# Optimization experiments

Measured on AMD Instinct MI355X. Metric: run time of the kernel, lower is better.

The kernel has to match this reference:

```python
import jax, jax.numpy as jnp
import numpy as np

CROP_H, CROP_W = 14, 14
EXTRAP = 0.0


def setup_inputs() -> dict:
    key = jax.random.key(0)
    k1, k2, k3 = jax.random.split(key, 3)
    image = jax.random.normal(k1, (8, 256, 200, 200), dtype=jnp.float32)
    boxes = jax.random.uniform(k2, (512, 4), dtype=jnp.float32)  # normalized [y1,x1,y2,x2]
    box_indices = jax.random.randint(k3, (512,), 0, 8).astype(jnp.int32)
    return {"image": image, "boxes": boxes, "box_indices": box_indices}


def _crop_and_resize(image, boxes, box_indices, crop_h, crop_w, extrap):
    # TF-style crop_and_resize with bilinear sampling (matches crop_and_resize_cpu).
    B, C, H, W = image.shape
    N = boxes.shape[0]
    y1, x1, y2, x2 = boxes[:, 0], boxes[:, 1], boxes[:, 2], boxes[:, 3]
    h_scale = (y2 - y1) * (H - 1) / (crop_h - 1)
    w_scale = (x2 - x1) * (W - 1) / (crop_w - 1)
    in_y = y1[:, None] * (H - 1) + jnp.arange(crop_h, dtype=jnp.float32)[None, :] * h_scale[:, None]  # [N,ch]
    in_x = x1[:, None] * (W - 1) + jnp.arange(crop_w, dtype=jnp.float32)[None, :] * w_scale[:, None]  # [N,cw]
    valid_y = (in_y >= 0) & (in_y <= H - 1)  # [N,ch]
    valid_x = (in_x >= 0) & (in_x <= W - 1)  # [N,cw]

    y_floor = jnp.floor(in_y)
    x_floor = jnp.floor(in_x)
    ly = (in_y - y_floor)[:, :, None, None]  # [N,ch,1,1]
    lx = (in_x - x_floor)[:, None, :, None]  # [N,1,cw,1]
    y0 = jnp.clip(y_floor, 0, H - 1).astype(jnp.int32)
    y1i = jnp.clip(jnp.ceil(in_y), 0, H - 1).astype(jnp.int32)
    x0 = jnp.clip(x_floor, 0, W - 1).astype(jnp.int32)
    x1i = jnp.clip(jnp.ceil(in_x), 0, W - 1).astype(jnp.int32)

    b = box_indices.astype(jnp.int32)[:, None, None]  # [N,1,1]

    def gather(yi, xi):
        # advanced indices [N,ch,cw] separated by ':' slice -> result [N,ch,cw,C]
        return image[b, :, yi[:, :, None], xi[:, None, :]]

    tl = gather(y0, x0)
    tr = gather(y0, x1i)
    bl = gather(y1i, x0)
    br = gather(y1i, x1i)

    top = tl + (tr - tl) * lx
    bot = bl + (br - bl) * lx
    val = top + (bot - top) * ly  # [N,ch,cw,C]

    mask = (valid_y[:, :, None] & valid_x[:, None, :])[:, :, :, None]
    val = jnp.where(mask, val, jnp.float32(extrap))
    return jnp.transpose(val, (0, 3, 1, 2))  # [N,C,ch,cw]


def reference(image, boxes, box_indices):
    return _crop_and_resize(image, boxes, box_indices, CROP_H, CROP_W, EXTRAP)
```

## Files before the change

### kernel.cpp

```cpp
#include <hip/hip_runtime.h>

#define CROP_H 14
#define CROP_W 14
#define NBOX   512
#define CH     256
#define IMH    200
#define IMW    200
#define PER_BOX (CH * CROP_H * CROP_W)
#define BLOCKS_PER_BOX (PER_BOX / 256)

__global__ __launch_bounds__(256) void CropAndResize_60146722013533_kernel(
    const float* __restrict__ image,
    const float* __restrict__ boxes,
    const int*   __restrict__ box_idx,
    float*       __restrict__ out)
{
    const int n = blockIdx.x;
    const int t = threadIdx.x;

    __shared__ int   sy0[CROP_H], sy1[CROP_H], sx0[CROP_W], sx1[CROP_W];
    __shared__ float sly[CROP_H], slx[CROP_W];
    __shared__ int   svy[CROP_H], svx[CROP_W];
    __shared__ int   sb;

    if (t < CROP_H + CROP_W) {
        const float by1 = boxes[n * 4 + 0];
        const float bx1 = boxes[n * 4 + 1];
        const float by2 = boxes[n * 4 + 2];
        const float bx2 = boxes[n * 4 + 3];
        if (t < CROP_H) {
            const int gy = t;
            float h_scale = (by2 - by1) * (float)(IMH - 1) / (float)(CROP_H - 1);
            float in_y = by1 * (float)(IMH - 1) + (float)gy * h_scale;
            svy[gy] = (in_y >= 0.0f && in_y <= (float)(IMH - 1)) ? 1 : 0;
            float yf = floorf(in_y);
            sly[gy] = in_y - yf;
            sy0[gy] = (int)fminf(fmaxf(yf, 0.0f), (float)(IMH - 1));
            sy1[gy] = (int)fminf(fmaxf(ceilf(in_y), 0.0f), (float)(IMH - 1));
        } else {
            const int gx = t - CROP_H;
            float w_scale = (bx2 - bx1) * (float)(IMW - 1) / (float)(CROP_W - 1);
            float in_x = bx1 * (float)(IMW - 1) + (float)gx * w_scale;
            svx[gx] = (in_x >= 0.0f && in_x <= (float)(IMW - 1)) ? 1 : 0;
            float xf = floorf(in_x);
            slx[gx] = in_x - xf;
            sx0[gx] = (int)fminf(fmaxf(xf, 0.0f), (float)(IMW - 1));
            sx1[gx] = (int)fminf(fmaxf(ceilf(in_x), 0.0f), (float)(IMW - 1));
        }
    }
    if (t == 0) sb = box_idx[n];
    __syncthreads();

    const int elem = blockIdx.y * 256 + t;
    const int c  = elem / (CROP_H * CROP_W);
    const int r  = elem - c * (CROP_H * CROP_W);
    const int gy = r / CROP_W;
    const int gx = r - gy * CROP_W;

    const float* base = image + ((size_t)(sb * CH + c)) * (size_t)(IMH * IMW);
    const int y0  = sy0[gy];
    const int y1i = sy1[gy];
    const int x0  = sx0[gx];
    const int x1i = sx1[gx];
    const float ly = sly[gy];
    const float lx = slx[gx];

    const int xb = (x0 < IMW - 2) ? x0 : (IMW - 2);
    const float* rowt = base + y0  * IMW + xb;
    const float* rowb = base + y1i * IMW + xb;
    float2 vt, vb;
    __builtin_memcpy(&vt, rowt, 8);
    __builtin_memcpy(&vb, rowb, 8);

    const float tl = (x0  == xb) ? vt.x : vt.y;
    const float tr = (x1i == xb) ? vt.x : vt.y;
    const float bl = (x0  == xb) ? vb.x : vb.y;
    const float br = (x1i == xb) ? vb.x : vb.y;

    const float top = tl + (tr - tl) * lx;
    const float bot = bl + (br - bl) * lx;
    float val = top + (bot - top) * ly;
    if (!(svy[gy] & svx[gx])) val = 0.0f;

    out[(size_t)n * PER_BOX + elem] = val;
}

extern "C" void kernel_launch(void* const* d_in, const int* in_sizes, int n_in,
                              void* d_out, int out_size, void* d_ws, size_t ws_size,
                              hipStream_t stream) {
    const float* image   = (const float*)d_in[0];
    const float* boxes   = (const float*)d_in[1];
    const int*   box_idx = (const int*)d_in[2];
    float* out = (float*)d_out;

    dim3 grid(NBOX, BLOCKS_PER_BOX, 1);
    dim3 block(256, 1, 1);
    CropAndResize_60146722013533_kernel<<<grid, block, 0, stream>>>(image, boxes, box_idx, out);
}
```

Measured before the change: 493.0 us.

## Sort boxes by image for L2 locality and process four outputs per thread

Adds a small prologue kernel that counting-sorts boxes by image index and interleaves them so concurrently scheduled blocks tend to share an image, aiming to improve cache reuse of gathered pixels. Each thread now handles four output elements with batched loads for more memory-level parallelism. Outputs are written with nontemporal stores to avoid polluting cache. The change adds an extra kernel launch, uses the workspace buffer, and raises register use.

New measurement: 493.2 us. Within noise of the previous version (+0.0%).

```diff
diff --git a/kernel.cpp b/kernel.cpp
--- a/kernel.cpp
+++ b/kernel.cpp
@@ -3,19 +3,52 @@
 #define CROP_H 14
 #define CROP_W 14
 #define NBOX   512
+#define NIMG   8
 #define CH     256
 #define IMH    200
 #define IMW    200
-#define PER_BOX (CH * CROP_H * CROP_W)
-#define BLOCKS_PER_BOX (PER_BOX / 256)
+#define PLANE   (IMH * IMW)
+#define NPOS    (CROP_H * CROP_W)
+#define PER_BOX (CH * NPOS)
+#define EPT     4
+#define CHUNK   (256 * EPT)
+#define NCHUNKS (PER_BOX / CHUNK)
 
-__global__ __launch_bounds__(256) void CropAndResize_60146722013533_kernel(
+__global__ __launch_bounds__(NBOX) void CropAndResize_perm_kernel(
+    const int* __restrict__ box_idx, int* __restrict__ perm)
+{
+    __shared__ int cnt[NIMG], base[NIMG], off[NIMG];
+    __shared__ int sorted[NBOX];
+    const int t = threadIdx.x;
+    if (t < NIMG) { cnt[t] = 0; off[t] = 0; }
+    __syncthreads();
+
+    const int img = box_idx[t];
+    atomicAdd(&cnt[img], 1);
+    __syncthreads();
+
+    if (t == 0) {
+        int s = 0;
+        #pragma unroll
+        for (int j = 0; j < NIMG; ++j) { base[j] = s; s += cnt[j]; }
+    }
+    __syncthreads();
+
+    const int r = base[img] + atomicAdd(&off[img], 1);
+    sorted[r] = t;
+    __syncthreads();
+
+    perm[t] = sorted[((t & 7) << 6) + (t >> 3)];
+}
+
+__global__ __launch_bounds__(256, 8) void CropAndResize_60146722013533_kernel(
     const float* __restrict__ image,
     const float* __restrict__ boxes,
     const int*   __restrict__ box_idx,
+    const int*   __restrict__ perm,
     float*       __restrict__ out)
 {
-    const int n = blockIdx.x;
+    const int n = perm[blockIdx.x];
     const int t = threadIdx.x;
 
     __shared__ int   sy0[CROP_H], sy1[CROP_H], sx0[CROP_W], sx1[CROP_W];
@@ -51,38 +84,54 @@
     if (t == 0) sb = box_idx[n];
     __syncthreads();
 
-    const int elem = blockIdx.y * 256 + t;
-    const int c  = elem / (CROP_H * CROP_W);
-    const int r  = elem - c * (CROP_H * CROP_W);
-    const int gy = r / CROP_W;
-    const int gx = r - gy * CROP_W;
+    const int base = blockIdx.y * CHUNK;
+    const float* __restrict__ img = image + (size_t)sb * CH * PLANE;
+    float* __restrict__ ob = out + (size_t)n * PER_BOX + base + t;
 
-    const float* base = image + ((size_t)(sb * CH + c)) * (size_t)(IMH * IMW);
-    const int y0  = sy0[gy];
-    const int y1i = sy1[gy];
-    const int x0  = sx0[gx];
-    const int x1i = sx1[gx];
-    const float ly = sly[gy];
-    const float lx = slx[gx];
+    const float* rt[EPT];
+    const float* rb[EPT];
+    int   xa[EPT], xbn[EPT], x1v[EPT], vm[EPT];
+    float lyv[EPT], lxv[EPT];
 
-    const int xb = (x0 < IMW - 2) ? x0 : (IMW - 2);
-    const float* rowt = base + y0  * IMW + xb;
-    const float* rowb = base + y1i * IMW + xb;
-    float2 vt, vb;
-    __builtin_memcpy(&vt, rowt, 8);
-    __builtin_memcpy(&vb, rowb, 8);
+    #pragma unroll
+    for (int k = 0; k < EPT; ++k) {
+        const int elem = base + t + 256 * k;
+        const int c  = elem / NPOS;
+        const int r  = elem - c * NPOS;
+        const int gy = r / CROP_W;
+        const int gx = r - gy * CROP_W;
+        const int x0 = sx0[gx];
+        const int xb = (x0 < IMW - 2) ? x0 : (IMW - 2);
+        const float* p = img + (size_t)c * PLANE;
+        rt[k]  = p + sy0[gy] * IMW + xb;
+        rb[k]  = p + sy1[gy] * IMW + xb;
+        xa[k]  = x0;
+        xbn[k] = xb;
+        x1v[k] = sx1[gx];
+        vm[k]  = svy[gy] & svx[gx];
+        lyv[k] = sly[gy];
+        lxv[k] = slx[gx];
+    }
 
-    const float tl = (x0  == xb) ? vt.x : vt.y;
-    const float tr = (x1i == xb) ? vt.x : vt.y;
-    const float bl = (x0  == xb) ? vb.x : vb.y;
-    const float br = (x1i == xb) ? vb.x : vb.y;
+    float2 vt[EPT], vb[EPT];
+    #pragma unroll
+    for (int k = 0; k < EPT; ++k) {
+        __builtin_memcpy(&vt[k], rt[k], 8);
+        __builtin_memcpy(&vb[k], rb[k], 8);
+    }
 
-    const float top = tl + (tr - tl) * lx;
-    const float bot = bl + (br - bl) * lx;
-    float val = top + (bot - top) * ly;
-    if (!(svy[gy] & svx[gx])) val = 0.0f;
-
-    out[(size_t)n * PER_BOX + elem] = val;
+    #pragma unroll
+    for (int k = 0; k < EPT; ++k) {
+        const float tl = (xa[k]  == xbn[k]) ? vt[k].x : vt[k].y;
+        const float tr = (x1v[k] == xbn[k]) ? vt[k].x : vt[k].y;
+        const float bl = (xa[k]  == xbn[k]) ? vb[k].x : vb[k].y;
+        const float br = (x1v[k] == xbn[k]) ? vb[k].x : vb[k].y;
+        const float top = tl + (tr - tl) * lxv[k];
+        const float bot = bl + (br - bl) * lxv[k];
+        float val = top + (bot - top) * lyv[k];
+        if (!vm[k]) val = 0.0f;
+        __builtin_nontemporal_store(val, ob + 256 * k);
+    }
 }
 
 extern "C" void kernel_launch(void* const* d_in, const int* in_sizes, int n_in,
@@ -91,9 +140,14 @@
     const float* image   = (const float*)d_in[0];
     const float* boxes   = (const float*)d_in[1];
     const int*   box_idx = (const int*)d_in[2];
-    float* out = (float*)d_out;
+    float* out  = (float*)d_out;
+    int*   perm = (int*)d_ws;
 
-    dim3 grid(NBOX, BLOCKS_PER_BOX, 1);
+    CropAndResize_perm_kernel<<<dim3(1, 1, 1), dim3(NBOX, 1, 1), 0, stream>>>(
+        box_idx, perm);
+
+    dim3 grid(NBOX, NCHUNKS, 1);
     dim3 block(256, 1, 1);
-    CropAndResize_60146722013533_kernel<<<grid, block, 0, stream>>>(image, boxes, box_idx, out);
+    CropAndResize_60146722013533_kernel<<<grid, block, 0, stream>>>(
+        image, boxes, box_idx, perm, out);
 }
```
